# Performance work log

Hardware: AMD Instinct MI355X
Metric: run time of the kernel (lower is better)

## Reference

```python
import jax, jax.numpy as jnp
import numpy as np

N_NODES = 100000


def gcn_conv(x, edge_index, W, b, num_nodes):
    # PyG GCNConv: h = X W; out = D^-1/2 (A+I) D^-1/2 h + b
    h = x @ W
    src, dst = edge_index[0], edge_index[1]
    loop = jnp.arange(num_nodes, dtype=edge_index.dtype)
    src = jnp.concatenate([src, loop])
    dst = jnp.concatenate([dst, loop])
    ew = jnp.ones(src.shape[0], dtype=x.dtype)  # edge_weight=None -> ones
    deg = jax.ops.segment_sum(ew, dst, num_segments=num_nodes)
    dinv = jnp.where(deg > 0, jax.lax.rsqrt(deg), 0.0)
    norm = dinv[src] * ew * dinv[dst]  # [E+N]
    msg = h[src] * norm[:, None]       # gather + scale
    out = jax.ops.segment_sum(msg, dst, num_segments=num_nodes)
    return out + b


def setup_inputs() -> dict:
    key = jax.random.key(0)
    k1, k2, k3, k4 = jax.random.split(key, 4)
    in_c, hid = 128, 128
    x = jax.random.normal(k1, (N_NODES, in_c), dtype=jnp.float32)
    edge_index = jax.random.randint(k2, (2, 1600000), 0, N_NODES, dtype=jnp.int64)
    s = 1.0 / np.sqrt(in_c)
    W1 = jax.random.uniform(k3, (in_c, hid), jnp.float32, -s, s)
    b1 = jnp.zeros((hid,), jnp.float32)
    W2 = jax.random.uniform(k4, (hid, hid), jnp.float32, -s, s)
    b2 = jnp.zeros((hid,), jnp.float32)
    return {"x": x, "edge_index": edge_index, "W1": W1, "b1": b1, "W2": W2, "b2": b2}


def reference(x, edge_index, W1, b1, W2, b2):
    h1 = jax.nn.relu(gcn_conv(x, edge_index, W1, b1, N_NODES))
    h2 = jax.nn.relu(gcn_conv(h1, edge_index, W2, b2, N_NODES))
    return jnp.concatenate([h1, h2], axis=1)  # [N, 2*hidden]
```

## Files before the change

### kernel.cpp

```cpp
#include <hip/hip_runtime.h>
#include <hip/hip_bf16.h>


#define FEAT 128
#define HW 64

typedef __attribute__((ext_vector_type(8))) short short8;
typedef __attribute__((ext_vector_type(4))) float f32x4;

static __device__ inline unsigned pack_bf16(float a, float b) {
    unsigned ua = __float_as_uint(a), ub = __float_as_uint(b);
    ua = (ua + 0x7fff + ((ua >> 16) & 1)) >> 16;
    ub = (ub + 0x7fff + ((ub >> 16) & 1)) >> 16;
    return (ua & 0xffffu) | (ub << 16);
}

static __device__ inline void split2(float x, unsigned short* hi, unsigned short* lo) {
    unsigned u = __float_as_uint(x);
    unsigned uh = (u + 0x7fff + ((u >> 16) & 1)) & 0xffff0000u;
    *hi = (unsigned short)(uh >> 16);
    float lo_f = x - __uint_as_float(uh);
    unsigned ul = __float_as_uint(lo_f);
    *lo = (unsigned short)((ul + 0x7fff + ((ul >> 16) & 1)) >> 16);
}


__global__ void pos_kernel(const int* __restrict__ dst, int E,
                           int* __restrict__ cnt, int* __restrict__ pos) {
    int e = blockIdx.x * 256 + threadIdx.x;
    if (e < E) pos[e] = atomicAdd(&cnt[dst[e]], 1);
}

__global__ __launch_bounds__(1024) void scan_block_kernel(
    const int* __restrict__ cnt, int* __restrict__ incl,
    int* __restrict__ bsum, float* __restrict__ dinv, int N) {
    __shared__ int s[1024];
    int tid = threadIdx.x;
    int i = blockIdx.x * 1024 + tid;
    int v = (i < N) ? cnt[i] : 0;
    if (i < N) dinv[i] = rsqrtf((float)(v + 1));
    s[tid] = v;
    __syncthreads();
    for (int off = 1; off < 1024; off <<= 1) {
        int add = (tid >= off) ? s[tid - off] : 0;
        __syncthreads();
        s[tid] += add;
        __syncthreads();
    }
    if (i < N) incl[i] = s[tid];
    if (tid == 1023) bsum[blockIdx.x] = s[1023];
}

__global__ __launch_bounds__(128) void scan_bsum_kernel(int* __restrict__ bsum, int NB) {
    __shared__ int s[128];
    int tid = threadIdx.x;
    int v = (tid < NB) ? bsum[tid] : 0;
    s[tid] = v;
    __syncthreads();
    for (int off = 1; off < 128; off <<= 1) {
        int add = (tid >= off) ? s[tid - off] : 0;
        __syncthreads();
        s[tid] += add;
        __syncthreads();
    }
    if (tid < NB) bsum[tid] = s[tid] - v;
}

__global__ void scan_finalize_kernel(const int* __restrict__ incl,
                                     const int* __restrict__ bsum,
                                     int* __restrict__ rowptr, int N) {
    int i = blockIdx.x * 256 + threadIdx.x;
    if (i < N) rowptr[i + 1] = incl[i] + bsum[i >> 10];
    if (i == 0) rowptr[0] = 0;
}

__global__ void scatter_kernel(const int* __restrict__ src, const int* __restrict__ dst,
                               const int* __restrict__ pos, const int* __restrict__ rowptr,
                               int* __restrict__ csr_src, int E) {
    int t = blockIdx.x * 256 + threadIdx.x;
    int stride = gridDim.x * 256;
    int E4 = E >> 2;
    const int4* s4 = (const int4*)src;
    const int4* d4 = (const int4*)dst;
    const int4* p4 = (const int4*)pos;
    for (int i = t; i < E4; i += stride) {
        int4 d = d4[i], s = s4[i], p = p4[i];
        csr_src[rowptr[d.x] + p.x] = s.x;
        csr_src[rowptr[d.y] + p.y] = s.y;
        csr_src[rowptr[d.z] + p.z] = s.z;
        csr_src[rowptr[d.w] + p.w] = s.w;
    }
    for (int e = E4 * 4 + t; e < E; e += stride) {
        csr_src[rowptr[dst[e]] + pos[e]] = src[e];
    }
}


__global__ void prep_w_kernel(const float* __restrict__ W1, const float* __restrict__ W2,
                              unsigned short* __restrict__ wf1_hi, unsigned short* __restrict__ wf1_lo,
                              unsigned short* __restrict__ wf2_hi, unsigned short* __restrict__ wf2_lo) {
    int g = blockIdx.x * 256 + threadIdx.x;
    int f = g & 16383;
    int j = f & 7, lane = (f >> 3) & 63, t = (f >> 9) & 7, ks = f >> 12;
    int k = ks * 32 + (lane >> 4) * 8 + j;
    int n = t * 16 + (lane & 15);
    unsigned short hi, lo;
    if (g < 16384) {
        split2(W1[k * 128 + n], &hi, &lo);
        wf1_hi[f] = hi; wf1_lo[f] = lo;
    } else {
        split2(W2[k * 128 + n], &hi, &lo);
        wf2_hi[f] = hi; wf2_lo[f] = lo;
    }
}


__global__ __launch_bounds__(256) void gemm_mfma_kernel(const float* __restrict__ X, int ldx,
    const unsigned short* __restrict__ wf_hi, const unsigned short* __restrict__ wf_lo,
    unsigned* __restrict__ H, int M) {
    __shared__ unsigned short xs_hi[64 * 128];
    __shared__ unsigned short xs_lo[64 * 128];
    int tid = threadIdx.x;
    int row0 = blockIdx.x * 64;

#pragma unroll
    for (int i = 0; i < 8; ++i) {
        int idx = tid + i * 256;
        int r = idx >> 5, c4 = (idx & 31) * 4;
        int gr = row0 + r;
        float4 v = make_float4(0.f, 0.f, 0.f, 0.f);
        if (gr < M) v = *(const float4*)(X + (size_t)gr * ldx + c4);
        unsigned short h4[4], l4[4];
        split2(v.x, &h4[0], &l4[0]); split2(v.y, &h4[1], &l4[1]);
        split2(v.z, &h4[2], &l4[2]); split2(v.w, &h4[3], &l4[3]);
        int sidx = r * 128 + (c4 ^ ((r & 7) << 3));
        uint2 ph, pl;
        ph.x = (unsigned)h4[0] | ((unsigned)h4[1] << 16);
        ph.y = (unsigned)h4[2] | ((unsigned)h4[3] << 16);
        pl.x = (unsigned)l4[0] | ((unsigned)l4[1] << 16);
        pl.y = (unsigned)l4[2] | ((unsigned)l4[3] << 16);
        *(uint2*)(xs_hi + sidx) = ph;
        *(uint2*)(xs_lo + sidx) = pl;
    }
    __syncthreads();

    int wave = tid >> 6, lane = tid & 63;
    int arow = wave * 16 + (lane & 15);
    int kgrp = (lane >> 4) * 8;

    f32x4 acc[8];
#pragma unroll
    for (int t = 0; t < 8; ++t) acc[t] = (f32x4){0.f, 0.f, 0.f, 0.f};

#pragma unroll
    for (int ks = 0; ks < 4; ++ks) {
        int k0 = ks * 32 + kgrp;
        int aidx = arow * 128 + (k0 ^ ((arow & 7) << 3));
        short8 a_hi = *(const short8*)(xs_hi + aidx);
        short8 a_lo = *(const short8*)(xs_lo + aidx);
        const unsigned short* bp = wf_hi + ((size_t)(ks * 8) * 64 + lane) * 8;
        const unsigned short* bq = wf_lo + ((size_t)(ks * 8) * 64 + lane) * 8;
#pragma unroll
        for (int t = 0; t < 8; ++t) {
            short8 b_hi = *(const short8*)(bp + t * 512);
            short8 b_lo = *(const short8*)(bq + t * 512);
            acc[t] = __builtin_amdgcn_mfma_f32_16x16x32_bf16(a_hi, b_hi, acc[t], 0, 0, 0);
            acc[t] = __builtin_amdgcn_mfma_f32_16x16x32_bf16(a_hi, b_lo, acc[t], 0, 0, 0);
            acc[t] = __builtin_amdgcn_mfma_f32_16x16x32_bf16(a_lo, b_hi, acc[t], 0, 0, 0);
        }
    }

    int rbase = row0 + wave * 16 + (lane >> 4) * 4;
    int c = lane & 15;
#pragma unroll
    for (int r = 0; r < 4; ++r) {
        int gr = rbase + r;
        if (gr < M) {
#pragma unroll
            for (int j = 0; j < 4; ++j) {
                H[(size_t)gr * HW + j * 16 + c] = pack_bf16(acc[2 * j][r], acc[2 * j + 1][r]);
            }
        }
    }
}


__global__ __launch_bounds__(256) void aggregate_kernel(const unsigned* __restrict__ H,
    const float* __restrict__ dinv, const int* __restrict__ rowptr,
    const int* __restrict__ csr_src, const float* __restrict__ bias,
    float* __restrict__ out, int ldo, int coloff, int N) {
    int node = blockIdx.x * 4 + (threadIdx.x >> 6);
    if (node >= N) return;
    int lane = threadIdx.x & 63;
    int f0 = 32 * (lane >> 4) + (lane & 15), f1 = f0 + 16;

    float di = dinv[node];
    float ax, ay;
    {
        unsigned v = H[(size_t)node * HW + lane];
        ax = __uint_as_float(v << 16) * di;
        ay = __uint_as_float(v & 0xffff0000u) * di;
    }

    int e0 = rowptr[node], e1 = rowptr[node + 1];
    int e = e0;
    for (; e + 7 < e1; e += 8) {
        int s[8]; float ws[8]; unsigned v[8];
#pragma unroll
        for (int i = 0; i < 8; ++i) s[i] = csr_src[e + i];
#pragma unroll
        for (int i = 0; i < 8; ++i) ws[i] = dinv[s[i]];
#pragma unroll
        for (int i = 0; i < 8; ++i) v[i] = H[(size_t)s[i] * HW + lane];
#pragma unroll
        for (int i = 0; i < 8; ++i) {
            ax = fmaf(__uint_as_float(v[i] << 16), ws[i], ax);
            ay = fmaf(__uint_as_float(v[i] & 0xffff0000u), ws[i], ay);
        }
    }
    for (; e + 3 < e1; e += 4) {
        int s[4]; float ws[4]; unsigned v[4];
#pragma unroll
        for (int i = 0; i < 4; ++i) s[i] = csr_src[e + i];
#pragma unroll
        for (int i = 0; i < 4; ++i) ws[i] = dinv[s[i]];
#pragma unroll
        for (int i = 0; i < 4; ++i) v[i] = H[(size_t)s[i] * HW + lane];
#pragma unroll
        for (int i = 0; i < 4; ++i) {
            ax = fmaf(__uint_as_float(v[i] << 16), ws[i], ax);
            ay = fmaf(__uint_as_float(v[i] & 0xffff0000u), ws[i], ay);
        }
    }
    for (; e < e1; ++e) {
        int s = csr_src[e];
        float ws = dinv[s];
        unsigned v = H[(size_t)s * HW + lane];
        ax = fmaf(__uint_as_float(v << 16), ws, ax);
        ay = fmaf(__uint_as_float(v & 0xffff0000u), ws, ay);
    }

    ax = fmaxf(ax * di + bias[f0], 0.f);
    ay = fmaxf(ay * di + bias[f1], 0.f);
    float* orow = out + (size_t)node * ldo + coloff;
    orow[f0] = ax;
    orow[f1] = ay;
}


extern "C" void kernel_launch(void* const* d_in, const int* in_sizes, int n_in,
                              void* d_out, int out_size, void* d_ws, size_t ws_size,
                              hipStream_t stream) {
    const float* x  = (const float*)d_in[0];
    const int*   ei = (const int*)d_in[1];
    const float* W1 = (const float*)d_in[2];
    const float* b1 = (const float*)d_in[3];
    const float* W2 = (const float*)d_in[4];
    const float* b2 = (const float*)d_in[5];
    float* out = (float*)d_out;

    const int N = in_sizes[0] / FEAT;
    const int E = in_sizes[1] / 2;
    const int* srcs = ei;
    const int* dsts = ei + E;

    const int NB = (N + 1023) / 1024;

    char* w = (char*)d_ws;
    unsigned* hb  = (unsigned*)w; w += (size_t)N * HW * sizeof(unsigned);
    float* dinv   = (float*)w; w += (size_t)N * sizeof(float);
    int*   cnt    = (int*)w;   w += (size_t)N * sizeof(int);
    int*   rowptr = (int*)w;   w += (size_t)(N + 4) * sizeof(int);
    int*   csr    = (int*)w;   w += (size_t)E * sizeof(int);
    int*   pos    = (int*)w;   w += (size_t)E * sizeof(int);
    int*   incl   = (int*)w;   w += (size_t)N * sizeof(int);
    int*   bsum   = (int*)w;   w += 128 * sizeof(int);
    unsigned short* wf1_hi = (unsigned short*)w; w += 16384 * sizeof(unsigned short);
    unsigned short* wf1_lo = (unsigned short*)w; w += 16384 * sizeof(unsigned short);
    unsigned short* wf2_hi = (unsigned short*)w; w += 16384 * sizeof(unsigned short);
    unsigned short* wf2_lo = (unsigned short*)w; w += 16384 * sizeof(unsigned short);

    hipMemsetAsync(cnt, 0, (size_t)N * sizeof(int), stream);

    int eg = (E + 255) / 256;
    int ng = (N + 255) / 256;
    prep_w_kernel<<<128, 256, 0, stream>>>(W1, W2, wf1_hi, wf1_lo, wf2_hi, wf2_lo);
    pos_kernel<<<eg, 256, 0, stream>>>(dsts, E, cnt, pos);
    scan_block_kernel<<<NB, 1024, 0, stream>>>(cnt, incl, bsum, dinv, N);
    scan_bsum_kernel<<<1, 128, 0, stream>>>(bsum, NB);
    scan_finalize_kernel<<<ng, 256, 0, stream>>>(incl, bsum, rowptr, N);
    scatter_kernel<<<1024, 256, 0, stream>>>(srcs, dsts, pos, rowptr, csr, E);

    int gg = (N + 63) / 64;
    int ag = (N + 3) / 4;
    gemm_mfma_kernel<<<gg, 256, 0, stream>>>(x, FEAT, wf1_hi, wf1_lo, hb, N);
    aggregate_kernel<<<ag, 256, 0, stream>>>(hb, dinv, rowptr, csr, b1, out, 2 * FEAT, 0, N);
    gemm_mfma_kernel<<<gg, 256, 0, stream>>>(out, 2 * FEAT, wf2_hi, wf2_lo, hb, N);
    aggregate_kernel<<<ag, 256, 0, stream>>>(hb, dinv, rowptr, csr, b2, out, 2 * FEAT, FEAT, N);
}
```

Measured before the change: 439.8 us.

## Vectorize pos atomics, load GEMM A directly, split aggregate edges across half-waves

The pos kernel becomes a grid-stride loop that reads four destination indices at once as int4 and issues four atomics per thread. The GEMM drops its LDS staging of X and loads each lane's A fragment straight from global memory, splitting it to hi/lo bf16 in registers. The aggregation kernel splits each wave into two halves that process alternating edges with 8-byte row loads, then combines the halves with a cross-lane shuffle. Together these aim to cut instruction count, raise memory-level parallelism in the gather, and remove LDS traffic and a barrier. The cost is less coalesced global A reads in the GEMM and half the lanes sitting idle during the final writeback.

New measurement: 450.2 us. +2.4%, slower.

```diff
diff --git a/kernel.cpp b/kernel.cpp
--- a/kernel.cpp
+++ b/kernel.cpp
@@ -24,11 +24,29 @@
     *lo = (unsigned short)((ul + 0x7fff + ((ul >> 16) & 1)) >> 16);
 }
 
+static __device__ inline float bl(unsigned v) { return __uint_as_float(v << 16); }
+static __device__ inline float bh(unsigned v) { return __uint_as_float(v & 0xffff0000u); }
+
 
 __global__ void pos_kernel(const int* __restrict__ dst, int E,
                            int* __restrict__ cnt, int* __restrict__ pos) {
-    int e = blockIdx.x * 256 + threadIdx.x;
-    if (e < E) pos[e] = atomicAdd(&cnt[dst[e]], 1);
+    int t = blockIdx.x * 256 + threadIdx.x;
+    int stride = gridDim.x * 256;
+    int E4 = E >> 2;
+    const int4* d4 = (const int4*)dst;
+    int4* p4 = (int4*)pos;
+    for (int i = t; i < E4; i += stride) {
+        int4 d = d4[i];
+        int4 p;
+        p.x = atomicAdd(&cnt[d.x], 1);
+        p.y = atomicAdd(&cnt[d.y], 1);
+        p.z = atomicAdd(&cnt[d.z], 1);
+        p.w = atomicAdd(&cnt[d.w], 1);
+        p4[i] = p;
+    }
+    for (int e = E4 * 4 + t; e < E; e += stride) {
+        pos[e] = atomicAdd(&cnt[dst[e]], 1);
+    }
 }
 
 __global__ __launch_bounds__(1024) void scan_block_kernel(
@@ -118,34 +136,12 @@
 __global__ __launch_bounds__(256) void gemm_mfma_kernel(const float* __restrict__ X, int ldx,
     const unsigned short* __restrict__ wf_hi, const unsigned short* __restrict__ wf_lo,
     unsigned* __restrict__ H, int M) {
-    __shared__ unsigned short xs_hi[64 * 128];
-    __shared__ unsigned short xs_lo[64 * 128];
     int tid = threadIdx.x;
+    int wave = tid >> 6, lane = tid & 63;
     int row0 = blockIdx.x * 64;
-
-#pragma unroll
-    for (int i = 0; i < 8; ++i) {
-        int idx = tid + i * 256;
-        int r = idx >> 5, c4 = (idx & 31) * 4;
-        int gr = row0 + r;
-        float4 v = make_float4(0.f, 0.f, 0.f, 0.f);
-        if (gr < M) v = *(const float4*)(X + (size_t)gr * ldx + c4);
-        unsigned short h4[4], l4[4];
-        split2(v.x, &h4[0], &l4[0]); split2(v.y, &h4[1], &l4[1]);
-        split2(v.z, &h4[2], &l4[2]); split2(v.w, &h4[3], &l4[3]);
-        int sidx = r * 128 + (c4 ^ ((r & 7) << 3));
-        uint2 ph, pl;
-        ph.x = (unsigned)h4[0] | ((unsigned)h4[1] << 16);
-        ph.y = (unsigned)h4[2] | ((unsigned)h4[3] << 16);
-        pl.x = (unsigned)l4[0] | ((unsigned)l4[1] << 16);
-        pl.y = (unsigned)l4[2] | ((unsigned)l4[3] << 16);
-        *(uint2*)(xs_hi + sidx) = ph;
-        *(uint2*)(xs_lo + sidx) = pl;
-    }
-    __syncthreads();
-
-    int wave = tid >> 6, lane = tid & 63;
-    int arow = wave * 16 + (lane & 15);
+    int arow = row0 + wave * 16 + (lane & 15);
+    int crow = (arow < M) ? arow : (M - 1);
+    const float* xrow = X + (size_t)crow * ldx;
     int kgrp = (lane >> 4) * 8;
 
     f32x4 acc[8];
@@ -155,9 +151,16 @@
 #pragma unroll
     for (int ks = 0; ks < 4; ++ks) {
         int k0 = ks * 32 + kgrp;
-        int aidx = arow * 128 + (k0 ^ ((arow & 7) << 3));
-        short8 a_hi = *(const short8*)(xs_hi + aidx);
-        short8 a_lo = *(const short8*)(xs_lo + aidx);
+        float4 xa = *(const float4*)(xrow + k0);
+        float4 xb = *(const float4*)(xrow + k0 + 4);
+        unsigned short h8[8], l8[8];
+        split2(xa.x, &h8[0], &l8[0]); split2(xa.y, &h8[1], &l8[1]);
+        split2(xa.z, &h8[2], &l8[2]); split2(xa.w, &h8[3], &l8[3]);
+        split2(xb.x, &h8[4], &l8[4]); split2(xb.y, &h8[5], &l8[5]);
+        split2(xb.z, &h8[6], &l8[6]); split2(xb.w, &h8[7], &l8[7]);
+        short8 a_hi, a_lo;
+#pragma unroll
+        for (int j = 0; j < 8; ++j) { a_hi[j] = (short)h8[j]; a_lo[j] = (short)l8[j]; }
         const unsigned short* bp = wf_hi + ((size_t)(ks * 8) * 64 + lane) * 8;
         const unsigned short* bq = wf_lo + ((size_t)(ks * 8) * 64 + lane) * 8;
 #pragma unroll
@@ -192,59 +195,60 @@
     int node = blockIdx.x * 4 + (threadIdx.x >> 6);
     if (node >= N) return;
     int lane = threadIdx.x & 63;
-    int f0 = 32 * (lane >> 4) + (lane & 15), f1 = f0 + 16;
+    int half = lane >> 5;
+    int li = lane & 31;
+    int w0 = 2 * li, w1 = 2 * li + 1;
 
     float di = dinv[node];
-    float ax, ay;
-    {
-        unsigned v = H[(size_t)node * HW + lane];
-        ax = __uint_as_float(v << 16) * di;
-        ay = __uint_as_float(v & 0xffff0000u) * di;
+    float a0x = 0.f, a0y = 0.f, a1x = 0.f, a1y = 0.f;
+    if (half == 0) {
+        uint2 v = *(const uint2*)(H + (size_t)node * HW + w0);
+        a0x = bl(v.x) * di; a0y = bh(v.x) * di;
+        a1x = bl(v.y) * di; a1y = bh(v.y) * di;
     }
 
     int e0 = rowptr[node], e1 = rowptr[node + 1];
-    int e = e0;
-    for (; e + 7 < e1; e += 8) {
-        int s[8]; float ws[8]; unsigned v[8];
-#pragma unroll
-        for (int i = 0; i < 8; ++i) s[i] = csr_src[e + i];
-#pragma unroll
-        for (int i = 0; i < 8; ++i) ws[i] = dinv[s[i]];
-#pragma unroll
-        for (int i = 0; i < 8; ++i) v[i] = H[(size_t)s[i] * HW + lane];
-#pragma unroll
-        for (int i = 0; i < 8; ++i) {
-            ax = fmaf(__uint_as_float(v[i] << 16), ws[i], ax);
-            ay = fmaf(__uint_as_float(v[i] & 0xffff0000u), ws[i], ay);
+    int e = e0 + half;
+    for (; e + 6 < e1; e += 8) {
+        int s[4]; float ws[4]; uint2 v[4];
+#pragma unroll
+        for (int i = 0; i < 4; ++i) s[i] = csr_src[e + 2 * i];
+#pragma unroll
+        for (int i = 0; i < 4; ++i) ws[i] = dinv[s[i]];
+#pragma unroll
+        for (int i = 0; i < 4; ++i) v[i] = *(const uint2*)(H + (size_t)s[i] * HW + w0);
+#pragma unroll
+        for (int i = 0; i < 4; ++i) {
+            a0x = fmaf(bl(v[i].x), ws[i], a0x);
+            a0y = fmaf(bh(v[i].x), ws[i], a0y);
+            a1x = fmaf(bl(v[i].y), ws[i], a1x);
+            a1y = fmaf(bh(v[i].y), ws[i], a1y);
         }
     }
-    for (; e + 3 < e1; e += 4) {
-        int s[4]; float ws[4]; unsigned v[4];
-#pragma unroll
-        for (int i = 0; i < 4; ++i) s[i] = csr_src[e + i];
-#pragma unroll
-        for (int i = 0; i < 4; ++i) ws[i] = dinv[s[i]];
-#pragma unroll
-        for (int i = 0; i < 4; ++i) v[i] = H[(size_t)s[i] * HW + lane];
-#pragma unroll
-        for (int i = 0; i < 4; ++i) {
-            ax = fmaf(__uint_as_float(v[i] << 16), ws[i], ax);
-            ay = fmaf(__uint_as_float(v[i] & 0xffff0000u), ws[i], ay);
-        }
-    }
-    for (; e < e1; ++e) {
+    for (; e < e1; e += 2) {
         int s = csr_src[e];
         float ws = dinv[s];
-        unsigned v = H[(size_t)s * HW + lane];
-        ax = fmaf(__uint_as_float(v << 16), ws, ax);
-        ay = fmaf(__uint_as_float(v & 0xffff0000u), ws, ay);
-    }
-
-    ax = fmaxf(ax * di + bias[f0], 0.f);
-    ay = fmaxf(ay * di + bias[f1], 0.f);
-    float* orow = out + (size_t)node * ldo + coloff;
-    orow[f0] = ax;
-    orow[f1] = ay;
+        uint2 v = *(const uint2*)(H + (size_t)s * HW + w0);
+        a0x = fmaf(bl(v.x), ws, a0x);
+        a0y = fmaf(bh(v.x), ws, a0y);
+        a1x = fmaf(bl(v.y), ws, a1x);
+        a1y = fmaf(bh(v.y), ws, a1y);
+    }
+
+    a0x += __shfl_xor(a0x, 32);
+    a0y += __shfl_xor(a0y, 32);
+    a1x += __shfl_xor(a1x, 32);
+    a1y += __shfl_xor(a1y, 32);
+
+    if (half == 0) {
+        float* orow = out + (size_t)node * ldo + coloff;
+        int f0 = 32 * (w0 >> 4) + (w0 & 15);
+        int g0 = 32 * (w1 >> 4) + (w1 & 15);
+        orow[f0]      = fmaxf(a0x * di + bias[f0], 0.f);
+        orow[f0 + 16] = fmaxf(a0y * di + bias[f0 + 16], 0.f);
+        orow[g0]      = fmaxf(a1x * di + bias[g0], 0.f);
+        orow[g0 + 16] = fmaxf(a1y * di + bias[g0 + 16], 0.f);
+    }
 }
 
 
@@ -282,10 +286,9 @@
 
     hipMemsetAsync(cnt, 0, (size_t)N * sizeof(int), stream);
 
-    int eg = (E + 255) / 256;
     int ng = (N + 255) / 256;
     prep_w_kernel<<<128, 256, 0, stream>>>(W1, W2, wf1_hi, wf1_lo, wf2_hi, wf2_lo);
-    pos_kernel<<<eg, 256, 0, stream>>>(dsts, E, cnt, pos);
+    pos_kernel<<<1024, 256, 0, stream>>>(dsts, E, cnt, pos);
     scan_block_kernel<<<NB, 1024, 0, stream>>>(cnt, incl, bsum, dinv, N);
     scan_bsum_kernel<<<1, 128, 0, stream>>>(bsum, NB);
     scan_finalize_kernel<<<ng, 256, 0, stream>>>(incl, bsum, rowptr, N);
```
